# Optimization experiments

Measured on AMD Instinct MI355X. Metric: run time of the kernel, lower is better.

The kernel has to match this reference:

```python
import jax, jax.numpy as jnp
import numpy as np

B, L, DIN, DQ, DS, DP = 16, 2048, 1024, 128, 64, 32

def _lin(k, din, dout):
    k1, k2 = jax.random.split(k)
    s = 1.0 / np.sqrt(din)
    W = jax.random.uniform(k1, (din, dout), jnp.float32, -s, s)
    b = jax.random.uniform(k2, (dout,), jnp.float32, -s, s)
    return W, b

def setup_inputs() -> dict:
    key = jax.random.key(0)
    ks = jax.random.split(key, 13)
    Wq, bq = _lin(ks[0], DIN, DQ)
    Wk, bk = _lin(ks[1], DIN, DQ)
    Wv, bv = _lin(ks[2], DIN, DQ)
    W1, b1 = _lin(ks[3], DS + DP, 128)
    W2, b2 = _lin(ks[4], 128, DQ)
    Wqc, bqc = _lin(ks[5], DQ, DQ)
    Wkc, bkc = _lin(ks[6], DQ, DQ)
    return dict(
        query=jax.random.normal(ks[7], (B, L, DIN), jnp.float32),
        key=jax.random.normal(ks[8], (B, L, DIN), jnp.float32),
        value=jax.random.normal(ks[9], (B, L, DIN), jnp.float32),
        sf=jax.random.normal(ks[10], (B, DS), jnp.float32),
        pos=jax.random.normal(ks[11], (L, DP), jnp.float32),
        Wq=Wq, bq=bq, Wk=Wk, bk=bk, Wv=Wv, bv=bv,
        W1=W1, b1=b1, W2=W2, b2=b2,
        Wqc=Wqc, bqc=bqc, Wkc=Wkc, bkc=bkc,
    )

def reference(query, key, value, sf, pos,
              Wq, bq, Wk, bk, Wv, bv,
              W1, b1, W2, b2, Wqc, bqc, Wkc, bkc):
    b, l, _ = query.shape
    q = query @ Wq + bq            # [b, l, dq]
    k = key @ Wk + bk              # [b, l, dq]
    v = value @ Wv + bv            # [b, l, dq]
    # CPE bias branch (pos is not None)
    sf_exp = jnp.broadcast_to(sf[:, None, :], (b, l, sf.shape[1]))
    pos_exp = jnp.broadcast_to(pos[None, :, :], (b, l, pos.shape[1]))
    cpe = jnp.concatenate([sf_exp, pos_exp], axis=2)         # [b, l, ds+32]
    cpe = jax.nn.relu(cpe @ W1 + b1) @ W2 + b2               # [b, l, dq]
    qc = cpe @ Wqc + bqc
    kc = cpe @ Wkc + bkc
    bias = jnp.einsum('bld,bmd->blm', qc, kc)                # [b, l, l]
    # add_mode == 0: post-softmax additive bias
    scale = jnp.sqrt(jnp.asarray(q.shape[-1], q.dtype))
    scores = jnp.einsum('bld,bmd->blm', q, k) / scale
    attn = jax.nn.softmax(scores, axis=-1) + bias
    out = jnp.einsum('blm,bmd->bld', attn, v)
    # L1 diff-norm regularizer over bias (use_cls=False)
    norm3 = (jnp.sum(jnp.abs(bias[:, 1:, :] - bias[:, :-1, :])) +
             jnp.sum(jnp.abs(bias[:, :, 1:] - bias[:, :, :-1])))
    return out, norm3
```

## Files before the change

kernel.cpp:

```cpp
#include <hip/hip_runtime.h>
#include <hip/hip_bf16.h>

typedef __attribute__((ext_vector_type(8))) short short8;
typedef __attribute__((ext_vector_type(4))) short short4x;
typedef __attribute__((ext_vector_type(4))) float floatx4;

#define MFMA16(a,b,c) __builtin_amdgcn_mfma_f32_16x16x32_bf16((a),(b),(c),0,0,0)

__device__ __forceinline__ unsigned short f2bf(float f) {
  unsigned int x = __float_as_uint(f);
  return (unsigned short)((x + 0x7fffu + ((x >> 16) & 1u)) >> 16);
}
__device__ __forceinline__ float bf2f(unsigned short s) {
  return __uint_as_float(((unsigned int)s) << 16);
}

__global__ __launch_bounds__(256)
void prep_kernel(const float* __restrict__ Wq, const float* __restrict__ Wk,
                 const float* __restrict__ Wv, const float* __restrict__ W1,
                 const float* __restrict__ b1, const float* __restrict__ W2,
                 const float* __restrict__ b2, const float* __restrict__ Wqc,
                 const float* __restrict__ bqc, const float* __restrict__ Wkc,
                 const float* __restrict__ bkc, const float* __restrict__ sf,
                 const float* __restrict__ pos,
                 unsigned short* __restrict__ Wf, unsigned short* __restrict__ Ut,
                 float* __restrict__ cqck, float* __restrict__ Asf,
                 float* __restrict__ Ppos)
{
  int blk = blockIdx.x, t = threadIdx.x;
  if (blk < 24) {
    int mat = blk >> 3, cg = blk & 7;
    const float* W = (mat == 0) ? Wq : (mat == 1) ? Wk : Wv;
    int l = t & 63, jp = t >> 6;
    int col = cg * 16 + (l & 15);
    unsigned short* o = Wf + (size_t)mat * 131072 + (size_t)cg * 32 * 512 + l * 8 + jp * 2;
    for (int ks = 0; ks < 32; ++ks) {
      int k = ks * 32 + (l >> 4) * 8 + jp * 2;
      o[ks * 512 + 0] = f2bf(W[(size_t)k * 128 + col]);
      o[ks * 512 + 1] = f2bf(W[(size_t)(k + 1) * 128 + col]);
    }
  } else if (blk >= 384 && blk < 512) {
    int j = blk - 384;
    int k = t & 127;
    const float* Wc = (t < 128) ? Wqc : Wkc;
    float acc = 0.f;
    for (int h = 0; h < 128; ++h) acc += W2[k * 128 + h] * Wc[h * 128 + j];
    Ut[(size_t)((t < 128) ? j : 128 + j) * 128 + k] = f2bf(acc);
  } else if (blk == 512) {
    int j = t & 127;
    const float* Wc = (t < 128) ? Wqc : Wkc;
    const float* bc = (t < 128) ? bqc : bkc;
    float acc = bc[j];
    for (int k = 0; k < 128; ++k) acc += b2[k] * Wc[k * 128 + j];
    cqck[t] = acc;
  } else if (blk > 512 && blk < 529) {
    int b = blk - 513;
    if (t < 128) {
      float acc = 0.f;
      for (int i = 0; i < 64; ++i) acc += sf[b * 64 + i] * W1[i * 128 + t];
      Asf[b * 128 + t] = acc;
    }
  } else if (blk >= 529) {
    int l = blk - 529;
    if (t < 128) {
      float acc = b1[t];
      for (int i = 0; i < 32; ++i) acc += pos[l * 32 + i] * W1[(64 + i) * 128 + t];
      Ppos[l * 128 + t] = acc;
    }
  }
}

__global__ __launch_bounds__(256)
void proj_kernel(const float* __restrict__ X, const unsigned short* __restrict__ Wf,
                 const float* __restrict__ bias,
                 unsigned short* __restrict__ qo, unsigned short* __restrict__ ko,
                 unsigned short* __restrict__ vto, int which)
{
  __shared__ __align__(16) unsigned short X_lds[32 * 1032];

  int t = threadIdx.x;
  int w = t >> 6, l = t & 63;
  int rowbase = blockIdx.x * 32;
  const int lrow = l & 15, hi = l >> 4;

#pragma unroll
  for (int r = 0; r < 8; ++r) {
    int row = w * 8 + r;
    const float* src = X + (size_t)(rowbase + row) * 1024 + l * 4;
    unsigned short* dst = &X_lds[row * 1032 + l * 4];
#pragma unroll
    for (int i = 0; i < 4; ++i) {
      float4 v = *(const float4*)(src + i * 256);
      short4x s;
      s[0] = (short)f2bf(v.x); s[1] = (short)f2bf(v.y);
      s[2] = (short)f2bf(v.z); s[3] = (short)f2bf(v.w);
      *(short4x*)(dst + i * 256) = s;
    }
  }
  __syncthreads();

  const unsigned short* wp0 = Wf + (size_t)(w * 2) * 32 * 512 + l * 8;
  const unsigned short* wp1 = Wf + (size_t)(w * 2 + 1) * 32 * 512 + l * 8;
  const int xo0 = lrow * 1032 + hi * 8;
  const int xo1 = (lrow + 16) * 1032 + hi * 8;

  floatx4 acc[2][2];
#pragma unroll
  for (int i = 0; i < 2; ++i)
#pragma unroll
    for (int j = 0; j < 2; ++j) { acc[i][j][0]=0.f; acc[i][j][1]=0.f; acc[i][j][2]=0.f; acc[i][j][3]=0.f; }

#pragma unroll 4
  for (int ks = 0; ks < 32; ++ks) {
    short8 b0 = *(const short8*)(wp0 + ks * 512);
    short8 b1 = *(const short8*)(wp1 + ks * 512);
    short8 a0 = *(const short8*)&X_lds[xo0 + ks * 32];
    short8 a1 = *(const short8*)&X_lds[xo1 + ks * 32];
    acc[0][0] = MFMA16(a0, b0, acc[0][0]);
    acc[0][1] = MFMA16(a0, b1, acc[0][1]);
    acc[1][0] = MFMA16(a1, b0, acc[1][0]);
    acc[1][1] = MFMA16(a1, b1, acc[1][1]);
  }

#pragma unroll
  for (int mf = 0; mf < 2; ++mf)
#pragma unroll
    for (int nf = 0; nf < 2; ++nf) {
      int col = w * 32 + nf * 16 + lrow;
      float bb = bias[col];
#pragma unroll
      for (int j = 0; j < 4; ++j) {
        int grow = rowbase + mf * 16 + hi * 4 + j;
        float v = acc[mf][nf][j] + bb;
        if (which == 0) qo[(size_t)grow * 128 + col] = f2bf(v);
        else if (which == 1) ko[(size_t)grow * 128 + col] = f2bf(v);
        else {
          int b = grow >> 11, li = grow & 2047;
          vto[((size_t)b * 128 + col) * 2048 + li] = f2bf(v);
        }
      }
    }
}

__global__ __launch_bounds__(256)
void qckc_kernel(const float* __restrict__ Asf, const float* __restrict__ Ppos,
                 const unsigned short* __restrict__ Ut, const float* __restrict__ cqck,
                 unsigned short* __restrict__ qc, unsigned short* __restrict__ kc)
{
  __shared__ __align__(16) unsigned short hid[64 * 136];
  int t = threadIdx.x, w = t >> 6, l = t & 63;
  int lbase = blockIdx.x * 64;
  int b = lbase >> 11;
  const int lrow = l & 15, lk = (l >> 4) * 8;
  {
    int r = t >> 2, seg = (t & 3) * 32;
    const float* pp = Ppos + (size_t)((lbase + r) & 2047) * 128 + seg;
    const float* aa = Asf + b * 128 + seg;
    unsigned short* dst = hid + r * 136 + seg;
#pragma unroll
    for (int c = 0; c < 32; c += 4) {
      float4 p4 = *(const float4*)(pp + c);
      float4 a4 = *(const float4*)(aa + c);
      dst[c + 0] = f2bf(fmaxf(p4.x + a4.x, 0.f));
      dst[c + 1] = f2bf(fmaxf(p4.y + a4.y, 0.f));
      dst[c + 2] = f2bf(fmaxf(p4.z + a4.z, 0.f));
      dst[c + 3] = f2bf(fmaxf(p4.w + a4.w, 0.f));
    }
  }
  __syncthreads();
  short8 a[4];
#pragma unroll
  for (int ks = 0; ks < 4; ++ks)
    a[ks] = *(const short8*)&hid[(w * 16 + lrow) * 136 + ks * 32 + lk];
  floatx4 acc[16];
#pragma unroll
  for (int nf = 0; nf < 16; ++nf) { acc[nf][0]=0.f; acc[nf][1]=0.f; acc[nf][2]=0.f; acc[nf][3]=0.f; }
#pragma unroll
  for (int nf = 0; nf < 16; ++nf)
#pragma unroll
    for (int ks = 0; ks < 4; ++ks) {
      short8 bfr = *(const short8*)(Ut + (size_t)(nf * 16 + lrow) * 128 + ks * 32 + lk);
      acc[nf] = MFMA16(a[ks], bfr, acc[nf]);
    }
#pragma unroll
  for (int nf = 0; nf < 16; ++nf) {
    int col = nf * 16 + lrow;
    float bb = cqck[col];
#pragma unroll
    for (int j = 0; j < 4; ++j) {
      int grow = lbase + w * 16 + (l >> 4) * 4 + j;
      float v = acc[nf][j] + bb;
      if (col < 128) qc[(size_t)grow * 128 + col] = f2bf(v);
      else kc[(size_t)grow * 128 + (col - 128)] = f2bf(v);
    }
  }
}

__global__ __launch_bounds__(256)
void m2_partial_kernel(const unsigned short* __restrict__ vt,
                       const unsigned short* __restrict__ kc,
                       float* __restrict__ M2p)
{
  __shared__ __align__(16) unsigned short kct[128 * 40];
  int ks = blockIdx.x, b = blockIdx.y;
  int t = threadIdx.x, w = t >> 6, l = t & 63;
  const int lrow = l & 15, lk = (l >> 4) * 8;
  floatx4 acc[2][8];
#pragma unroll
  for (int i = 0; i < 2; ++i)
#pragma unroll
    for (int j = 0; j < 8; ++j) { acc[i][j][0]=0.f; acc[i][j][1]=0.f; acc[i][j][2]=0.f; acc[i][j][3]=0.f; }
  for (int mc = 0; mc < 8; ++mc) {
    int mbase = ks * 256 + mc * 32;
    {
      int mm = t & 31, ib = (t >> 5) * 16;
      const unsigned short* src = kc + ((size_t)b * 2048 + mbase + mm) * 128 + ib;
#pragma unroll
      for (int ii = 0; ii < 16; ++ii) kct[(ib + ii) * 40 + mm] = src[ii];
    }
    __syncthreads();
#pragma unroll
    for (int mf = 0; mf < 2; ++mf) {
      int jrow = w * 32 + mf * 16 + lrow;
      short8 a = *(const short8*)(vt + ((size_t)b * 128 + jrow) * 2048 + mbase + lk);
#pragma unroll
      for (int nf = 0; nf < 8; ++nf) {
        short8 bfr = *(const short8*)&kct[(nf * 16 + lrow) * 40 + lk];
        acc[mf][nf] = MFMA16(a, bfr, acc[mf][nf]);
      }
    }
    __syncthreads();
  }
#pragma unroll
  for (int mf = 0; mf < 2; ++mf)
#pragma unroll
    for (int nf = 0; nf < 8; ++nf)
#pragma unroll
      for (int j = 0; j < 4; ++j) {
        int jr = w * 32 + mf * 16 + (l >> 4) * 4 + j;
        int ic = nf * 16 + lrow;
        M2p[(((size_t)ks * 16 + b) * 128 + jr) * 128 + ic] = acc[mf][nf][j];
      }
}

__global__ void m2_reduce_kernel(const float* __restrict__ M2p, float* __restrict__ M2t)
{
  int idx = blockIdx.x * 256 + threadIdx.x;
  float s = 0.f;
#pragma unroll
  for (int ksp = 0; ksp < 8; ++ksp) s += M2p[(size_t)ksp * 262144 + idx];
  M2t[idx] = s;
}

__global__ __launch_bounds__(256)
void attn_kernel(const unsigned short* __restrict__ qbf, const unsigned short* __restrict__ kbf,
                 const unsigned short* __restrict__ vt, const unsigned short* __restrict__ qc,
                 const float* __restrict__ M2t, float* __restrict__ out)
{
  __shared__ __align__(16) unsigned short K_lds[64 * 136];
  __shared__ __align__(16) unsigned short V_lds[128 * 72];
  __shared__ __align__(16) unsigned short P_lds[4 * 16 * 72];
  int t = threadIdx.x, w = t >> 6, l = t & 63;
  int lbase = blockIdx.x * 64, b = blockIdx.y;
  const int lrow = l & 15, lk = (l >> 4) * 8;
  const float rscale2 = 0.08838834764831845f * 1.4426950408889634f;

  size_t browq = (size_t)b * 2048 + lbase + w * 16 + lrow;
  short8 aq[4];
#pragma unroll
  for (int ks = 0; ks < 4; ++ks)
    aq[ks] = *(const short8*)(qbf + browq * 128 + ks * 32 + lk);

  float m_run[4] = {-1e30f, -1e30f, -1e30f, -1e30f};
  float s_run[4] = {0.f, 0.f, 0.f, 0.f};
  floatx4 o[8];
#pragma unroll
  for (int nf = 0; nf < 8; ++nf) { o[nf][0]=0.f; o[nf][1]=0.f; o[nf][2]=0.f; o[nf][3]=0.f; }

  int sr = t >> 2, sseg = (t & 3) * 32;
  int vr = t >> 1, vseg = (t & 1) * 32;

  const short8* ksrc0 = (const short8*)(kbf + ((size_t)b * 2048 + sr) * 128 + sseg);
  const short8* vsrc0 = (const short8*)(vt + ((size_t)b * 128 + vr) * 2048 + vseg);

  short8 kr[4], vrg[4];
#pragma unroll
  for (int i = 0; i < 4; ++i) { kr[i] = ksrc0[i]; vrg[i] = vsrc0[i]; }

  for (int kt = 0; kt < 32; ++kt) {
    {
      short8* dst = (short8*)&K_lds[sr * 136 + sseg];
      dst[0] = kr[0]; dst[1] = kr[1]; dst[2] = kr[2]; dst[3] = kr[3];
      short8* vdst = (short8*)&V_lds[vr * 72 + vseg];
      vdst[0] = vrg[0]; vdst[1] = vrg[1]; vdst[2] = vrg[2]; vdst[3] = vrg[3];
    }
    __syncthreads();
    if (kt < 31) {
      const short8* ks2 = ksrc0 + (size_t)(kt + 1) * 1024;
      const short8* vs2 = vsrc0 + (size_t)(kt + 1) * 8;
#pragma unroll
      for (int i = 0; i < 4; ++i) { kr[i] = ks2[i]; vrg[i] = vs2[i]; }
    }
    floatx4 s[4];
    __builtin_amdgcn_s_setprio(1);
#pragma unroll
    for (int cf = 0; cf < 4; ++cf) {
      floatx4 a4; a4[0]=0.f; a4[1]=0.f; a4[2]=0.f; a4[3]=0.f;
#pragma unroll
      for (int ks = 0; ks < 4; ++ks) {
        short8 bfr = *(const short8*)&K_lds[(cf * 16 + lrow) * 136 + ks * 32 + lk];
        a4 = MFMA16(aq[ks], bfr, a4);
      }
      s[cf] = a4 * rscale2;
    }
    __builtin_amdgcn_s_setprio(0);
    float fmul[4];
#pragma unroll
    for (int j = 0; j < 4; ++j) {
      float tm = fmaxf(fmaxf(s[0][j], s[1][j]), fmaxf(s[2][j], s[3][j]));
#pragma unroll
      for (int off = 1; off < 16; off <<= 1) tm = fmaxf(tm, __shfl_xor(tm, off, 64));
      float nm = fmaxf(m_run[j], tm);
      float f = exp2f(m_run[j] - nm);
      m_run[j] = nm;
      float rs = 0.f;
#pragma unroll
      for (int cf = 0; cf < 4; ++cf) {
        float p = exp2f(s[cf][j] - nm);
        s[cf][j] = p;
        rs += p;
      }
#pragma unroll
      for (int off = 1; off < 16; off <<= 1) rs += __shfl_xor(rs, off, 64);
      s_run[j] = s_run[j] * f + rs;
      fmul[j] = f;
    }
#pragma unroll
    for (int nf = 0; nf < 8; ++nf)
#pragma unroll
      for (int j = 0; j < 4; ++j) o[nf][j] *= fmul[j];
    unsigned short* pw = P_lds + w * (16 * 72);
#pragma unroll
    for (int cf = 0; cf < 4; ++cf)
#pragma unroll
      for (int j = 0; j < 4; ++j)
        pw[((l >> 4) * 4 + j) * 72 + cf * 16 + lrow] = f2bf(s[cf][j]);
    __builtin_amdgcn_s_setprio(1);
#pragma unroll
    for (int kf = 0; kf < 2; ++kf) {
      short8 ap = *(const short8*)&pw[lrow * 72 + kf * 32 + lk];
#pragma unroll
      for (int nf = 0; nf < 8; ++nf) {
        short8 bv = *(const short8*)&V_lds[(nf * 16 + lrow) * 72 + kf * 32 + lk];
        o[nf] = MFMA16(ap, bv, o[nf]);
      }
    }
    __builtin_amdgcn_s_setprio(0);
    __syncthreads();
  }
#pragma unroll
  for (int nf = 0; nf < 8; ++nf)
#pragma unroll
    for (int j = 0; j < 4; ++j) o[nf][j] /= s_run[j];
#pragma unroll
  for (int ks = 0; ks < 4; ++ks) {
    short8 aqc = *(const short8*)(qc + browq * 128 + ks * 32 + lk);
#pragma unroll
    for (int nf = 0; nf < 8; ++nf) {
      const float* mp = M2t + ((size_t)b * 128 + nf * 16 + lrow) * 128 + ks * 32 + lk;
      float4 m0 = *(const float4*)(mp);
      float4 m1 = *(const float4*)(mp + 4);
      short8 bm;
      bm[0]=(short)f2bf(m0.x); bm[1]=(short)f2bf(m0.y); bm[2]=(short)f2bf(m0.z); bm[3]=(short)f2bf(m0.w);
      bm[4]=(short)f2bf(m1.x); bm[5]=(short)f2bf(m1.y); bm[6]=(short)f2bf(m1.z); bm[7]=(short)f2bf(m1.w);
      o[nf] = MFMA16(aqc, bm, o[nf]);
    }
  }
#pragma unroll
  for (int nf = 0; nf < 8; ++nf)
#pragma unroll
    for (int j = 0; j < 4; ++j) {
      int grow = lbase + w * 16 + (l >> 4) * 4 + j;
      out[((size_t)b * 2048 + grow) * 128 + nf * 16 + lrow] = o[nf][j];
    }
}

__global__ __launch_bounds__(256)
void norm_kernel(const unsigned short* __restrict__ qc, const unsigned short* __restrict__ kc,
                 float* __restrict__ partial)
{
  __shared__ __align__(16) unsigned short T1[129 * 136];
  __shared__ __align__(16) unsigned short T2[129 * 136];
  __shared__ float red[8];
  int t = threadIdx.x, w = t >> 6, l = t & 63;
  int ltm = blockIdx.x;
  int lt = ltm >> 4, mt = ltm & 15;
  int b = blockIdx.y;
  const int lrow = l & 15, lk = (l >> 4) * 8;
  {
    int r = t >> 1, half = (t & 1) * 64;
    const unsigned short* asrc = qc + ((size_t)b * 2048 + lt * 128 + r) * 128 + half;
    const unsigned short* bsrc = kc + ((size_t)b * 2048 + mt * 128 + r) * 128 + half;
    unsigned short* adst = T1 + r * 136 + half;
    unsigned short* bdst = T2 + r * 136 + half;
#pragma unroll
    for (int c = 0; c < 64; c += 8) {
      *(short8*)(adst + c) = *(const short8*)(asrc + c);
      *(short8*)(bdst + c) = *(const short8*)(bsrc + c);
    }
    if (t < 16) {
      int gr = lt * 128 + 128; if (gr > 2047) gr = 2047;
      *(short8*)(T1 + 128 * 136 + t * 8) =
          *(const short8*)(qc + ((size_t)b * 2048 + gr) * 128 + t * 8);
    } else if (t < 32) {
      int c = (t - 16) * 8;
      int gr = mt * 128 + 128; if (gr > 2047) gr = 2047;
      *(short8*)(T2 + 128 * 136 + c) =
          *(const short8*)(kc + ((size_t)b * 2048 + gr) * 128 + c);
    }
  }
  __syncthreads();
  floatx4 acc0[2][8], acc1[2][8];
#pragma unroll
  for (int i = 0; i < 2; ++i)
#pragma unroll
    for (int j = 0; j < 8; ++j) {
      acc0[i][j][0]=0.f; acc0[i][j][1]=0.f; acc0[i][j][2]=0.f; acc0[i][j][3]=0.f;
      acc1[i][j][0]=0.f; acc1[i][j][1]=0.f; acc1[i][j][2]=0.f; acc1[i][j][3]=0.f;
    }
#pragma unroll
  for (int ks = 0; ks < 4; ++ks) {
    int off = ks * 32 + lk;
    short8 ad[2], cd[2];
#pragma unroll
    for (int mf = 0; mf < 2; ++mf) {
      int r = w * 32 + mf * 16 + lrow;
      short8 x1 = *(const short8*)&T1[r * 136 + off];
      short8 y1 = *(const short8*)&T1[(r + 1) * 136 + off];
      short8 x2 = *(const short8*)&T2[r * 136 + off];
      short8 y2 = *(const short8*)&T2[(r + 1) * 136 + off];
      short8 d1, d2;
#pragma unroll
      for (int ii = 0; ii < 8; ++ii) {
        d1[ii] = (short)f2bf(bf2f((unsigned short)y1[ii]) - bf2f((unsigned short)x1[ii]));
        d2[ii] = (short)f2bf(bf2f((unsigned short)y2[ii]) - bf2f((unsigned short)x2[ii]));
      }
      ad[mf] = d1; cd[mf] = d2;
    }
#pragma unroll
    for (int nf = 0; nf < 8; ++nf) {
      short8 bk = *(const short8*)&T2[(nf * 16 + lrow) * 136 + off];
      short8 bq = *(const short8*)&T1[(nf * 16 + lrow) * 136 + off];
      acc0[0][nf] = MFMA16(ad[0], bk, acc0[0][nf]);
      acc0[1][nf] = MFMA16(ad[1], bk, acc0[1][nf]);
      acc1[0][nf] = MFMA16(cd[0], bq, acc1[0][nf]);
      acc1[1][nf] = MFMA16(cd[1], bq, acc1[1][nf]);
    }
  }
  float s0 = 0.f, s1 = 0.f;
#pragma unroll
  for (int i = 0; i < 2; ++i)
#pragma unroll
    for (int nf = 0; nf < 8; ++nf)
#pragma unroll
      for (int j = 0; j < 4; ++j) {
        s0 += fabsf(acc0[i][nf][j]);
        s1 += fabsf(acc1[i][nf][j]);
      }
#pragma unroll
  for (int off = 1; off < 64; off <<= 1) {
    s0 += __shfl_xor(s0, off, 64);
    s1 += __shfl_xor(s1, off, 64);
  }
  if (l == 0) { red[w] = s0; red[4 + w] = s1; }
  __syncthreads();
  if (t == 0) {
    partial[((size_t)0 * 16 + b) * 256 + ltm] = red[0] + red[1] + red[2] + red[3];
    partial[((size_t)1 * 16 + b) * 256 + ltm] = red[4] + red[5] + red[6] + red[7];
  }
}

__global__ void norm_reduce_kernel(const float* __restrict__ partial, float* __restrict__ outp)
{
  __shared__ float red[4];
  int t = threadIdx.x;
  float s = 0.f;
  for (int i = t; i < 8192; i += 256) s += partial[i];
#pragma unroll
  for (int off = 1; off < 64; off <<= 1) s += __shfl_xor(s, off, 64);
  if ((t & 63) == 0) red[t >> 6] = s;
  __syncthreads();
  if (t == 0) outp[0] = red[0] + red[1] + red[2] + red[3];
}

extern "C" void kernel_launch(void* const* d_in, const int* in_sizes, int n_in,
                              void* d_out, int out_size, void* d_ws, size_t ws_size,
                              hipStream_t stream)
{
  const float* query = (const float*)d_in[0];
  const float* key_  = (const float*)d_in[1];
  const float* value = (const float*)d_in[2];
  const float* sf    = (const float*)d_in[3];
  const float* pos   = (const float*)d_in[4];
  const float* Wq  = (const float*)d_in[5];  const float* bq  = (const float*)d_in[6];
  const float* Wk  = (const float*)d_in[7];  const float* bk  = (const float*)d_in[8];
  const float* Wv  = (const float*)d_in[9];  const float* bv  = (const float*)d_in[10];
  const float* W1  = (const float*)d_in[11]; const float* b1  = (const float*)d_in[12];
  const float* W2  = (const float*)d_in[13]; const float* b2  = (const float*)d_in[14];
  const float* Wqc = (const float*)d_in[15]; const float* bqc = (const float*)d_in[16];
  const float* Wkc = (const float*)d_in[17]; const float* bkc = (const float*)d_in[18];
  float* out = (float*)d_out;

  char* ws = (char*)d_ws;
  size_t off = 0;
  auto alloc = [&](size_t bytes) {
    char* p = ws + off;
    off += (bytes + 255) & ~(size_t)255;
    return p;
  };
  unsigned short* Wf   = (unsigned short*)alloc((size_t)3 * 131072 * 2);
  unsigned short* Ut   = (unsigned short*)alloc((size_t)256 * 128 * 2);
  float* cqck          = (float*)alloc(256 * 4);
  float* Asf           = (float*)alloc(16 * 128 * 4);
  float* Ppos          = (float*)alloc((size_t)2048 * 128 * 4);
  unsigned short* qbf  = (unsigned short*)alloc((size_t)32768 * 128 * 2);
  unsigned short* kbf  = (unsigned short*)alloc((size_t)32768 * 128 * 2);
  unsigned short* vt   = (unsigned short*)alloc((size_t)32768 * 128 * 2);
  unsigned short* qc   = (unsigned short*)alloc((size_t)32768 * 128 * 2);
  unsigned short* kc   = (unsigned short*)alloc((size_t)32768 * 128 * 2);
  float* M2p           = (float*)alloc((size_t)8 * 262144 * 4);
  float* M2t           = (float*)alloc((size_t)262144 * 4);
  float* npartial      = (float*)alloc((size_t)8192 * 4);
  (void)ws_size; (void)in_sizes; (void)n_in; (void)out_size;

  prep_kernel<<<2577, 256, 0, stream>>>(Wq, Wk, Wv, W1, b1, W2, b2, Wqc, bqc, Wkc, bkc,
                                        sf, pos, Wf, Ut, cqck, Asf, Ppos);
  proj_kernel<<<1024, 256, 0, stream>>>(query, Wf,          bq, qbf, kbf, vt, 0);
  proj_kernel<<<1024, 256, 0, stream>>>(key_,  Wf + 131072, bk, qbf, kbf, vt, 1);
  proj_kernel<<<1024, 256, 0, stream>>>(value, Wf + 262144, bv, qbf, kbf, vt, 2);
  qckc_kernel<<<512, 256, 0, stream>>>(Asf, Ppos, Ut, cqck, qc, kc);
  m2_partial_kernel<<<dim3(8, 16), 256, 0, stream>>>(vt, kc, M2p);
  m2_reduce_kernel<<<1024, 256, 0, stream>>>(M2p, M2t);
  attn_kernel<<<dim3(32, 16), 256, 0, stream>>>(qbf, kbf, vt, qc, M2t, out);
  norm_kernel<<<dim3(256, 16), 256, 0, stream>>>(qc, kc, npartial);
  norm_reduce_kernel<<<1, 256, 0, stream>>>(npartial, out + (size_t)4194304);
}
```

Baseline: 368.3 us.

## Fold softmax scale into Q projection and defer online-softmax rescaling

Folds the 1/sqrt(d)*log2(e) scale into the Q projection epilogue, so the attention loop no longer multiplies the scores. The online-softmax running max is now updated only when some row's tile max exceeds it by more than 8, which skips the rescale of the output accumulators in most iterations. It also uses the hardware bf16 convert instruction when packing P, and replaces the final per-element division with a multiply by a reciprocal. The risks are extra rounding from scaling q before bf16 quantization, and exp2 values up to 2^8 feeding into bf16 P and the fp32 sums.

```diff
diff --git a/kernel.cpp b/kernel.cpp
--- a/kernel.cpp
+++ b/kernel.cpp
@@ -13,6 +13,11 @@
 }
 __device__ __forceinline__ float bf2f(unsigned short s) {
   return __uint_as_float(((unsigned int)s) << 16);
+}
+__device__ __forceinline__ unsigned short f2bf_cvt(float f) {
+  unsigned int r;
+  asm("v_cvt_pk_bf16_f32 %0, %1, %1" : "=v"(r) : "v"(f));
+  return (unsigned short)r;
 }
 
 __global__ __launch_bounds__(256)
@@ -82,6 +87,7 @@
   int w = t >> 6, l = t & 63;
   int rowbase = blockIdx.x * 32;
   const int lrow = l & 15, hi = l >> 4;
+  const float RS2 = 0.08838834764831845f * 1.4426950408889634f;
 
 #pragma unroll
   for (int r = 0; r < 8; ++r) {
@@ -132,7 +138,7 @@
       for (int j = 0; j < 4; ++j) {
         int grow = rowbase + mf * 16 + hi * 4 + j;
         float v = acc[mf][nf][j] + bb;
-        if (which == 0) qo[(size_t)grow * 128 + col] = f2bf(v);
+        if (which == 0) qo[(size_t)grow * 128 + col] = f2bf(v * RS2);
         else if (which == 1) ko[(size_t)grow * 128 + col] = f2bf(v);
         else {
           int b = grow >> 11, li = grow & 2047;
@@ -263,7 +269,6 @@
   int t = threadIdx.x, w = t >> 6, l = t & 63;
   int lbase = blockIdx.x * 64, b = blockIdx.y;
   const int lrow = l & 15, lk = (l >> 4) * 8;
-  const float rscale2 = 0.08838834764831845f * 1.4426950408889634f;
 
   size_t browq = (size_t)b * 2048 + lbase + w * 16 + lrow;
   short8 aq[4];
@@ -311,40 +316,52 @@
         short8 bfr = *(const short8*)&K_lds[(cf * 16 + lrow) * 136 + ks * 32 + lk];
         a4 = MFMA16(aq[ks], bfr, a4);
       }
-      s[cf] = a4 * rscale2;
+      s[cf] = a4;
     }
     __builtin_amdgcn_s_setprio(0);
-    float fmul[4];
+    float tm[4];
 #pragma unroll
     for (int j = 0; j < 4; ++j) {
-      float tm = fmaxf(fmaxf(s[0][j], s[1][j]), fmaxf(s[2][j], s[3][j]));
-#pragma unroll
-      for (int off = 1; off < 16; off <<= 1) tm = fmaxf(tm, __shfl_xor(tm, off, 64));
-      float nm = fmaxf(m_run[j], tm);
-      float f = exp2f(m_run[j] - nm);
-      m_run[j] = nm;
+      float m0 = fmaxf(fmaxf(s[0][j], s[1][j]), fmaxf(s[2][j], s[3][j]));
+#pragma unroll
+      for (int off = 1; off < 16; off <<= 1) m0 = fmaxf(m0, __shfl_xor(m0, off, 64));
+      tm[j] = m0;
+    }
+    bool need = (tm[0] > m_run[0] + 8.f) | (tm[1] > m_run[1] + 8.f) |
+                (tm[2] > m_run[2] + 8.f) | (tm[3] > m_run[3] + 8.f);
+    if (__any(need)) {
+      float fmul[4];
+#pragma unroll
+      for (int j = 0; j < 4; ++j) {
+        float nm = fmaxf(m_run[j], tm[j]);
+        fmul[j] = exp2f(m_run[j] - nm);
+        m_run[j] = nm;
+        s_run[j] *= fmul[j];
+      }
+#pragma unroll
+      for (int nf = 0; nf < 8; ++nf)
+#pragma unroll
+        for (int j = 0; j < 4; ++j) o[nf][j] *= fmul[j];
+    }
+#pragma unroll
+    for (int j = 0; j < 4; ++j) {
       float rs = 0.f;
 #pragma unroll
       for (int cf = 0; cf < 4; ++cf) {
-        float p = exp2f(s[cf][j] - nm);
+        float p = exp2f(s[cf][j] - m_run[j]);
         s[cf][j] = p;
         rs += p;
       }
 #pragma unroll
       for (int off = 1; off < 16; off <<= 1) rs += __shfl_xor(rs, off, 64);
-      s_run[j] = s_run[j] * f + rs;
-      fmul[j] = f;
-    }
-#pragma unroll
-    for (int nf = 0; nf < 8; ++nf)
-#pragma unroll
-      for (int j = 0; j < 4; ++j) o[nf][j] *= fmul[j];
+      s_run[j] += rs;
+    }
     unsigned short* pw = P_lds + w * (16 * 72);
 #pragma unroll
     for (int cf = 0; cf < 4; ++cf)
 #pragma unroll
       for (int j = 0; j < 4; ++j)
-        pw[((l >> 4) * 4 + j) * 72 + cf * 16 + lrow] = f2bf(s[cf][j]);
+        pw[((l >> 4) * 4 + j) * 72 + cf * 16 + lrow] = f2bf_cvt(s[cf][j]);
     __builtin_amdgcn_s_setprio(1);
 #pragma unroll
     for (int kf = 0; kf < 2; ++kf) {
@@ -358,10 +375,13 @@
     __builtin_amdgcn_s_setprio(0);
     __syncthreads();
   }
+  float inv[4];
+#pragma unroll
+  for (int j = 0; j < 4; ++j) inv[j] = 1.f / s_run[j];
 #pragma unroll
   for (int nf = 0; nf < 8; ++nf)
 #pragma unroll
-    for (int j = 0; j < 4; ++j) o[nf][j] /= s_run[j];
+    for (int j = 0; j < 4; ++j) o[nf][j] *= inv[j];
 #pragma unroll
   for (int ks = 0; ks < 4; ++ks) {
     short8 aqc = *(const short8*)(qc + browq * 128 + ks * 32 + lk);
```

Result: faster. 358.9 us (-2.5%).
